# Kernel tuning notes

Measured on AMD Instinct MI355X. Metric: run time of the kernel, lower is better.

The kernel has to match this reference:

```python
import jax, jax.numpy as jnp
import numpy as np
from jax.ops import segment_sum, segment_max

N, F, H, HEADS, E, OUT = 50000, 256, 64, 4, 800000, 16


def setup_inputs() -> dict:
    key = jax.random.key(0)
    ks = jax.random.split(key, 16)
    s = 0.05
    return {
        "x": jax.random.normal(ks[0], (N, F), jnp.float32),
        "edge_index": jax.random.randint(ks[1], (2, E), 0, N, jnp.int64),
        # GCN layer params
        "W_gcn1": jax.random.normal(ks[2], (F, H), jnp.float32) * s,
        "b_gcn1": jnp.zeros((H,), jnp.float32),
        "W_gcn2": jax.random.normal(ks[3], (H, OUT), jnp.float32) * s,
        "b_gcn2": jnp.zeros((OUT,), jnp.float32),
        # GAT layer 1 (heads=HEADS, concat)
        "W_gat1": jax.random.normal(ks[4], (F, HEADS * H), jnp.float32) * s,
        "a_src1": jax.random.normal(ks[5], (HEADS, H), jnp.float32) * s,
        "a_dst1": jax.random.normal(ks[6], (HEADS, H), jnp.float32) * s,
        "b_gat1": jnp.zeros((HEADS * H,), jnp.float32),
        # GAT layer 2 (heads=1, concat=False)
        "W_gat2": jax.random.normal(ks[7], (HEADS * H, OUT), jnp.float32) * s,
        "a_src2": jax.random.normal(ks[8], (1, OUT), jnp.float32) * s,
        "a_dst2": jax.random.normal(ks[9], (1, OUT), jnp.float32) * s,
        "b_gat2": jnp.zeros((OUT,), jnp.float32),
    }


def _add_self_loops(edge_index, n):
    loop = jnp.arange(n, dtype=edge_index.dtype)
    src = jnp.concatenate([edge_index[0], loop])
    dst = jnp.concatenate([edge_index[1], loop])
    return src, dst


def _gcn(x, src, dst, norm, W, b, n):
    h = x @ W  # [N, out]
    out = segment_sum(h[src] * norm[:, None], dst, num_segments=n)
    return out + b


def _gat(x, src, dst, W, a_s, a_d, b, heads, concat, n):
    h = (x @ W).reshape(n, heads, -1)  # [N, heads, C]
    s_src = jnp.einsum("nhc,hc->nh", h, a_s)
    s_dst = jnp.einsum("nhc,hc->nh", h, a_d)
    e = jax.nn.leaky_relu(s_src[src] + s_dst[dst], 0.2)  # [Etot, heads]
    m = segment_max(e, dst, num_segments=n)               # per-dst softmax
    p = jnp.exp(e - m[dst])
    denom = segment_sum(p, dst, num_segments=n)
    alpha = p / denom[dst]
    out = segment_sum(h[src] * alpha[..., None], dst, num_segments=n)
    out = out.reshape(n, -1) if concat else out.mean(axis=1)
    return out + b


def reference(x, edge_index, W_gcn1, b_gcn1, W_gcn2, b_gcn2,
              W_gat1, a_src1, a_dst1, b_gat1,
              W_gat2, a_src2, a_dst2, b_gat2):
    n = x.shape[0]
    src, dst = _add_self_loops(edge_index, n)
    # symmetric GCN normalization on self-loop-augmented graph
    deg = segment_sum(jnp.ones_like(dst, x.dtype), dst, num_segments=n)
    dinv = jnp.where(deg > 0, jax.lax.rsqrt(deg), 0.0)
    norm = dinv[src] * dinv[dst]

    x_gcn = jax.nn.relu(_gcn(x, src, dst, norm, W_gcn1, b_gcn1, n))
    x_gcn = _gcn(x_gcn, src, dst, norm, W_gcn2, b_gcn2, n)

    x_gat = jax.nn.relu(_gat(x, src, dst, W_gat1, a_src1, a_dst1, b_gat1, HEADS, True, n))
    x_gat = _gat(x_gat, src, dst, W_gat2, a_src2, a_dst2, b_gat2, 1, False, n)

    return jnp.concatenate([x_gcn, x_gat], axis=1)
```

## Files before the change

kernel.cpp:

```cpp
#include <hip/hip_runtime.h>
#include <math.h>

#define NN     50000
#define FF     256
#define HH     64
#define NHEADS 4
#define EE     800000
#define OUTD   16

typedef __attribute__((ext_vector_type(8))) short short8;
typedef __attribute__((ext_vector_type(4))) float f32x4;

__device__ inline unsigned short f2bf(float f) {
    unsigned u = __builtin_bit_cast(unsigned, f);
    unsigned r = (u + 0x7fff + ((u >> 16) & 1)) >> 16;
    return (unsigned short)r;
}
__device__ inline float bf2f(unsigned short s) {
    unsigned u = ((unsigned)s) << 16;
    return __builtin_bit_cast(float, u);
}

__global__ void k_zero_int(int* __restrict__ p, int n) {
    int i = blockIdx.x * blockDim.x + threadIdx.x;
    if (i < n) p[i] = 0;
}

__global__ void k_count(const int* __restrict__ dst, int* __restrict__ cnt, int e) {
    int i = blockIdx.x * blockDim.x + threadIdx.x;
    if (i < e) atomicAdd(&cnt[dst[i]], 1);
}

__global__ __launch_bounds__(256) void k_scan_a(const int* __restrict__ cnt,
                                                int* __restrict__ partial, int n) {
    int i = blockIdx.x * 256 + threadIdx.x;
    int v = (i < n) ? cnt[i] : 0;
#pragma unroll
    for (int off = 32; off >= 1; off >>= 1) v += __shfl_xor(v, off, 64);
    __shared__ int ws[4];
    int wave = threadIdx.x >> 6;
    if ((threadIdx.x & 63) == 0) ws[wave] = v;
    __syncthreads();
    if (threadIdx.x == 0) partial[blockIdx.x] = ws[0] + ws[1] + ws[2] + ws[3];
}

__global__ __launch_bounds__(256) void k_scan_b(const int* __restrict__ partial,
                                                int* __restrict__ blockoff,
                                                int* __restrict__ total_out, int nb) {
    __shared__ int arr[256];
    int tid = threadIdx.x;
    arr[tid] = (tid < nb) ? partial[tid] : 0;
    __syncthreads();
#pragma unroll
    for (int off = 1; off < 256; off <<= 1) {
        int v = arr[tid];
        int add = (tid >= off) ? arr[tid - off] : 0;
        __syncthreads();
        arr[tid] = v + add;
        __syncthreads();
    }
    if (tid < nb) blockoff[tid] = arr[tid] - partial[tid];
    if (tid == 0) *total_out = arr[255];
}

__global__ __launch_bounds__(256) void k_scan_c(const int* __restrict__ cnt,
                                                const int* __restrict__ blockoff,
                                                int* __restrict__ row_start,
                                                int* __restrict__ cursor,
                                                float* __restrict__ dinv, int n) {
    __shared__ int arr[256];
    int tid = threadIdx.x;
    int i = blockIdx.x * 256 + tid;
    int c = (i < n) ? cnt[i] : 0;
    arr[tid] = c;
    __syncthreads();
#pragma unroll
    for (int off = 1; off < 256; off <<= 1) {
        int v = arr[tid];
        int add = (tid >= off) ? arr[tid - off] : 0;
        __syncthreads();
        arr[tid] = v + add;
        __syncthreads();
    }
    if (i < n) {
        int excl = arr[tid] - c + blockoff[blockIdx.x];
        row_start[i] = excl;
        cursor[i] = excl;
        dinv[i] = rsqrtf((float)(c + 1));
    }
}

__global__ void k_fill(const int* __restrict__ src, const int* __restrict__ dst,
                       int* __restrict__ cursor, int* __restrict__ col, int e) {
    int i = blockIdx.x * blockDim.x + threadIdx.x;
    if (i < e) {
        int d = dst[i];
        int pos = atomicAdd(&cursor[d], 1);
        col[pos] = src[i];
    }
}

__device__ inline void pack_one(const float* __restrict__ W,
                                unsigned short* __restrict__ bhi,
                                unsigned short* __restrict__ blo,
                                int t_, int NT, int NTOT, int TOFF, int SRC_NC) {
    int lane = t_ & 63;
    int tile = (t_ >> 6) % NT;
    int kb = (t_ >> 6) / NT;
    int q = lane >> 4, c = lane & 15;
    size_t off = ((size_t)(kb * NTOT + TOFF + tile) * 64 + lane) * 8;
#pragma unroll
    for (int j = 0; j < 8; j++) {
        float w = W[(size_t)(kb * 32 + q * 8 + j) * SRC_NC + tile * 16 + c];
        unsigned short h = f2bf(w);
        bhi[off + j] = h;
        if (blo) blo[off + j] = f2bf(w - bf2f(h));
    }
}

#define NTT 20
__global__ __launch_bounds__(256) void k_pack_all(const float* __restrict__ Wg1,
                                                  const float* __restrict__ Wgat1,
                                                  const float* __restrict__ Wg2,
                                                  const float* __restrict__ Wgat2,
                                                  unsigned short* __restrict__ bhiC,
                                                  unsigned short* __restrict__ bhiG2,
                                                  unsigned short* __restrict__ bloG2,
                                                  unsigned short* __restrict__ bhiA2,
                                                  unsigned short* __restrict__ bloA2) {
    int t = blockIdx.x * 256 + threadIdx.x;
    if (t < 2048)        pack_one(Wg1,   bhiC,  nullptr, t,         4,  NTT, 0, 64);
    else if (t < 10240)  pack_one(Wgat1, bhiC,  nullptr, t - 2048,  16, NTT, 4, 256);
    else if (t < 10368)  pack_one(Wg2,   bhiG2, bloG2,   t - 10240, 1,  1,   0, 16);
    else if (t < 10880)  pack_one(Wgat2, bhiA2, bloA2,   t - 10368, 1,  1,   0, 16);
}

__global__ __launch_bounds__(256) void mfma_gemm_fused(const float* __restrict__ A,
                                                       const unsigned short* __restrict__ Bhi,
                                                       unsigned short* __restrict__ Ch1,
                                                       unsigned short* __restrict__ Chg,
                                                       const float* __restrict__ dinv,
                                                       const float* __restrict__ a_s,
                                                       const float* __restrict__ a_d,
                                                       float* __restrict__ ssrc,
                                                       float* __restrict__ sdst,
                                                       int M) {
    const int K = 256;
    int tid = threadIdx.x;
    int w = tid >> 6, lane = tid & 63, q = lane >> 4, c = lane & 15;
    int row_base = blockIdx.x * 64 + w * 16;
    int ar = min(row_base + c, M - 1);
    const float* ap = A + (size_t)ar * K + q * 8;
    const short8* bp = (const short8*)Bhi + lane;

    f32x4 acc[NTT];
#pragma unroll
    for (int t = 0; t < NTT; t++) acc[t] = (f32x4){0.f, 0.f, 0.f, 0.f};

    for (int kb = 0; kb < 8; kb++) {
        float av[8];
        *(float4*)(av)     = *(const float4*)(ap + kb * 32);
        *(float4*)(av + 4) = *(const float4*)(ap + kb * 32 + 4);
        short8 ahi, alo;
#pragma unroll
        for (int j = 0; j < 8; j++) {
            unsigned short h = f2bf(av[j]);
            ahi[j] = (short)h;
            alo[j] = (short)f2bf(av[j] - bf2f(h));
        }
#pragma unroll
        for (int t = 0; t < NTT; t++) {
            short8 bhi = bp[(size_t)(kb * NTT + t) * 64];
            acc[t] = __builtin_amdgcn_mfma_f32_16x16x32_bf16(ahi, bhi, acc[t], 0, 0, 0);
            acc[t] = __builtin_amdgcn_mfma_f32_16x16x32_bf16(alo, bhi, acc[t], 0, 0, 0);
        }
    }

#pragma unroll
    for (int i = 0; i < 4; i++) {
        int r = row_base + q * 4 + i;
        float ss[4] = {0.f, 0.f, 0.f, 0.f};
        float sd[4] = {0.f, 0.f, 0.f, 0.f};
#pragma unroll
        for (int t = 0; t < 16; t++) {
            float v = acc[t + 4][i];
            ss[t >> 2] += v * a_s[t * 16 + c];
            sd[t >> 2] += v * a_d[t * 16 + c];
        }
#pragma unroll
        for (int h = 0; h < 4; h++) {
#pragma unroll
            for (int off = 1; off <= 8; off <<= 1) {
                ss[h] += __shfl_xor(ss[h], off, 16);
                sd[h] += __shfl_xor(sd[h], off, 16);
            }
        }
        if (c == i && r < M) {
            *(float4*)(ssrc + (size_t)r * 4) = make_float4(ss[0], ss[1], ss[2], ss[3]);
            *(float4*)(sdst + (size_t)r * 4) = make_float4(sd[0], sd[1], sd[2], sd[3]);
        }
    }

#pragma unroll
    for (int i = 0; i < 4; i++) {
        int r = row_base + q * 4 + i;
        if (r < M) {
            float sc = dinv[r];
#pragma unroll
            for (int t = 0; t < 4; t++)
                Ch1[(size_t)r * 64 + t * 16 + c] = f2bf(acc[t][i] * sc);
#pragma unroll
            for (int t = 0; t < 16; t++)
                Chg[(size_t)r * 256 + t * 16 + c] = f2bf(acc[t + 4][i]);
        }
    }
}

template <int KB, bool SCALE, bool SC2, int OFS>
__device__ inline void n16_body(int bx, int tid,
                                const unsigned short* __restrict__ A,
                                const unsigned short* __restrict__ Bhi,
                                const unsigned short* __restrict__ Blo,
                                unsigned short* __restrict__ Cbf,
                                const float* __restrict__ rowscale,
                                const float* __restrict__ a_s2,
                                const float* __restrict__ a_d2,
                                float* __restrict__ s2s,
                                float* __restrict__ s2d, int M) {
    const int K = KB * 32;
    int w = tid >> 6, lane = tid & 63, q = lane >> 4, c = lane & 15;
    int row_base = bx * 64 + w * 16;
    int ar = min(row_base + c, M - 1);
    const unsigned short* ap = A + (size_t)ar * K + q * 8;
    f32x4 acc = (f32x4){0.f, 0.f, 0.f, 0.f};
#pragma unroll
    for (int kb = 0; kb < KB; kb++) {
        short8 av = *(const short8*)(ap + kb * 32);
        size_t bo = ((size_t)kb * 64 + lane) * 8;
        short8 bh = *(const short8*)(Bhi + bo);
        short8 bl = *(const short8*)(Blo + bo);
        acc = __builtin_amdgcn_mfma_f32_16x16x32_bf16(av, bh, acc, 0, 0, 0);
        acc = __builtin_amdgcn_mfma_f32_16x16x32_bf16(av, bl, acc, 0, 0, 0);
    }
    if (SC2) {
#pragma unroll
        for (int i = 0; i < 4; i++) {
            float ps = acc[i] * a_s2[c];
            float pd = acc[i] * a_d2[c];
#pragma unroll
            for (int off = 1; off <= 8; off <<= 1) {
                ps += __shfl_xor(ps, off, 16);
                pd += __shfl_xor(pd, off, 16);
            }
            int r = row_base + q * 4 + i;
            if (c == i && r < M) {
                s2s[r] = ps;
                s2d[r] = pd;
            }
        }
    }
#pragma unroll
    for (int i = 0; i < 4; i++) {
        int r = row_base + q * 4 + i;
        if (r < M) {
            float sc = SCALE ? rowscale[r] : 1.0f;
            Cbf[((size_t)r * 16 + c) * 2 + OFS] = f2bf(acc[i] * sc);
        }
    }
}

__global__ __launch_bounds__(256) void mfma_n16_both(const unsigned short* __restrict__ Ag,
                                                     const unsigned short* __restrict__ Ac,
                                                     const unsigned short* __restrict__ bhiA2,
                                                     const unsigned short* __restrict__ bloA2,
                                                     const unsigned short* __restrict__ bhiG2,
                                                     const unsigned short* __restrict__ bloG2,
                                                     unsigned short* __restrict__ pairb,
                                                     const float* __restrict__ dinv,
                                                     const float* __restrict__ a_s2,
                                                     const float* __restrict__ a_d2,
                                                     float* __restrict__ s2s,
                                                     float* __restrict__ s2d,
                                                     int M, int GB) {
    int bx = blockIdx.x;
    if (bx < GB)
        n16_body<8, false, true, 1>(bx, threadIdx.x, Ag, bhiA2, bloA2, pairb,
                                    nullptr, a_s2, a_d2, s2s, s2d, M);
    else
        n16_body<2, true, false, 0>(bx - GB, threadIdx.x, Ac, bhiG2, bloG2, pairb,
                                    dinv, nullptr, nullptr, nullptr, nullptr, M);
}

__global__ __launch_bounds__(256) void both_agg(const unsigned short* __restrict__ hg,
                                                const unsigned short* __restrict__ h1,
                                                const int* __restrict__ rs,
                                                const int* __restrict__ col,
                                                const float* __restrict__ ssrc,
                                                const float* __restrict__ sdst,
                                                const float* __restrict__ dinv,
                                                const float* __restrict__ bgat,
                                                const float* __restrict__ bgcn,
                                                unsigned short* __restrict__ outg,
                                                unsigned short* __restrict__ outc) {
    __shared__ int s_lds[4][64];
    __shared__ float p_lds[4][64 * 4];
    int tid = threadIdx.x;
    int w = tid >> 6, lane = tid & 63;
    int wid = blockIdx.x * 4 + w;
    int hh = lane >> 4;
    int cidx = (lane & 15) * 4;
    int* sl = s_lds[w];
    float* pl = p_lds[w];

    float di = dinv[wid];
    float4 sd4 = *(const float4*)(sdst + (size_t)wid * 4);
    float sdv[4] = {sd4.x, sd4.y, sd4.z, sd4.w};
    float4 sf4 = *(const float4*)(ssrc + (size_t)wid * 4);
    float sfv[4] = {sf4.x, sf4.y, sf4.z, sf4.w};
    float psf[4];
#pragma unroll
    for (int h = 0; h < 4; h++) {
        float e = sfv[h] + sdv[h];
        e = (e >= 0.f) ? e : 0.2f * e;
        psf[h] = __expf(e);
    }
    float pse = (hh & 2) ? ((hh & 1) ? psf[3] : psf[2]) : ((hh & 1) ? psf[1] : psf[0]);
    const unsigned short* hbase = hg + lane * 4;
    ushort4 hvs = *(const ushort4*)(hbase + (size_t)wid * 256);
    float4 acc;
    acc.x = bf2f(hvs.x) * pse; acc.y = bf2f(hvs.y) * pse;
    acc.z = bf2f(hvs.z) * pse; acc.w = bf2f(hvs.w) * pse;
    float4 accc = make_float4(0.f, 0.f, 0.f, 0.f);

    float lsum[4] = {0.f, 0.f, 0.f, 0.f};
    int beg = rs[wid], end = rs[wid + 1];
    for (int j0 = beg; j0 < end; j0 += 64) {
        int cnt = min(64, end - j0);
        if (lane < cnt) {
            int sreg = col[j0 + lane];
            float4 sv = *(const float4*)(ssrc + (size_t)sreg * 4);
            float svv[4] = {sv.x, sv.y, sv.z, sv.w};
            float pv[4];
#pragma unroll
            for (int h = 0; h < 4; h++) {
                float e = svv[h] + sdv[h];
                e = (e >= 0.f) ? e : 0.2f * e;
                pv[h] = __expf(e);
                lsum[h] += pv[h];
            }
            sl[lane] = sreg;
            *(float4*)&pl[lane * 4] = make_float4(pv[0], pv[1], pv[2], pv[3]);
        }
        int e = 0;
        for (; e + 4 <= cnt; e += 4) {
            int s0 = sl[e], s1 = sl[e + 1], s2 = sl[e + 2], s3 = sl[e + 3];
            float p0 = pl[e * 4 + hh], p1 = pl[(e + 1) * 4 + hh];
            float p2 = pl[(e + 2) * 4 + hh], p3 = pl[(e + 3) * 4 + hh];
            ushort4 h0 = *(const ushort4*)(hbase + (size_t)s0 * 256);
            ushort4 h1v = *(const ushort4*)(hbase + (size_t)s1 * 256);
            ushort4 h2 = *(const ushort4*)(hbase + (size_t)s2 * 256);
            ushort4 h3 = *(const ushort4*)(hbase + (size_t)s3 * 256);
            acc.x += bf2f(h0.x) * p0; acc.y += bf2f(h0.y) * p0;
            acc.z += bf2f(h0.z) * p0; acc.w += bf2f(h0.w) * p0;
            acc.x += bf2f(h1v.x) * p1; acc.y += bf2f(h1v.y) * p1;
            acc.z += bf2f(h1v.z) * p1; acc.w += bf2f(h1v.w) * p1;
            acc.x += bf2f(h2.x) * p2; acc.y += bf2f(h2.y) * p2;
            acc.z += bf2f(h2.z) * p2; acc.w += bf2f(h2.w) * p2;
            acc.x += bf2f(h3.x) * p3; acc.y += bf2f(h3.y) * p3;
            acc.z += bf2f(h3.z) * p3; acc.w += bf2f(h3.w) * p3;
        }
        for (; e < cnt; e++) {
            int s = sl[e];
            float p = pl[e * 4 + hh];
            ushort4 hv = *(const ushort4*)(hbase + (size_t)s * 256);
            acc.x += bf2f(hv.x) * p; acc.y += bf2f(hv.y) * p;
            acc.z += bf2f(hv.z) * p; acc.w += bf2f(hv.w) * p;
        }
        int e2 = hh;
        for (; e2 + 4 < cnt; e2 += 8) {
            int sa = sl[e2], sb = sl[e2 + 4];
            ushort4 va = *(const ushort4*)(h1 + (size_t)sa * HH + cidx);
            ushort4 vb = *(const ushort4*)(h1 + (size_t)sb * HH + cidx);
            accc.x += bf2f(va.x) + bf2f(vb.x);
            accc.y += bf2f(va.y) + bf2f(vb.y);
            accc.z += bf2f(va.z) + bf2f(vb.z);
            accc.w += bf2f(va.w) + bf2f(vb.w);
        }
        if (e2 < cnt) {
            int sa = sl[e2];
            ushort4 va = *(const ushort4*)(h1 + (size_t)sa * HH + cidx);
            accc.x += bf2f(va.x); accc.y += bf2f(va.y);
            accc.z += bf2f(va.z); accc.w += bf2f(va.w);
        }
    }
#pragma unroll
    for (int h = 0; h < 4; h++) {
        float v = lsum[h];
        for (int off = 32; off >= 1; off >>= 1) v += __shfl_xor(v, off, 64);
        lsum[h] = v + psf[h];
    }
    float lt = (hh & 2) ? ((hh & 1) ? lsum[3] : lsum[2]) : ((hh & 1) ? lsum[1] : lsum[0]);
    float li = 1.0f / lt;
    float4 bv = *(const float4*)(bgat + lane * 4);
    ushort4 o;
    o.x = f2bf(fmaxf(acc.x * li + bv.x, 0.f));
    o.y = f2bf(fmaxf(acc.y * li + bv.y, 0.f));
    o.z = f2bf(fmaxf(acc.z * li + bv.z, 0.f));
    o.w = f2bf(fmaxf(acc.w * li + bv.w, 0.f));
    *(ushort4*)(outg + (size_t)wid * 256 + lane * 4) = o;
#pragma unroll
    for (int off = 16; off <= 32; off <<= 1) {
        accc.x += __shfl_xor(accc.x, off, 64);
        accc.y += __shfl_xor(accc.y, off, 64);
        accc.z += __shfl_xor(accc.z, off, 64);
        accc.w += __shfl_xor(accc.w, off, 64);
    }
    if (hh == 0) {
        ushort4 sv = *(const ushort4*)(h1 + (size_t)wid * HH + cidx);
        float4 bc = *(const float4*)(bgcn + cidx);
        ushort4 oc;
        oc.x = f2bf(fmaxf((accc.x + bf2f(sv.x)) * di + bc.x, 0.f));
        oc.y = f2bf(fmaxf((accc.y + bf2f(sv.y)) * di + bc.y, 0.f));
        oc.z = f2bf(fmaxf((accc.z + bf2f(sv.z)) * di + bc.z, 0.f));
        oc.w = f2bf(fmaxf((accc.w + bf2f(sv.w)) * di + bc.w, 0.f));
        *(ushort4*)(outc + (size_t)wid * HH + cidx) = oc;
    }
}

__global__ __launch_bounds__(256) void final_agg(const unsigned* __restrict__ hp,
                                                 const int* __restrict__ rs,
                                                 const int* __restrict__ col,
                                                 const float* __restrict__ dinv,
                                                 const float* __restrict__ s2s,
                                                 const float* __restrict__ s2d,
                                                 const float* __restrict__ bg2,
                                                 const float* __restrict__ bga2,
                                                 float* __restrict__ out) {
    int t = blockIdx.x * 256 + threadIdx.x;
    int node = t >> 4;
    int c = t & 15;
    float di = dinv[node];
    float sd = s2d[node];
    float es = s2s[node] + sd;
    es = (es >= 0.f) ? es : 0.2f * es;
    float psf = __expf(es);
    unsigned pvs = hp[(size_t)node * 16 + c];
    float accg = bf2f((unsigned short)pvs);
    float acca = bf2f((unsigned short)(pvs >> 16)) * psf;
    float lp = 0.f;
    int beg = rs[node], end = rs[node + 1];
    for (int j0 = beg; j0 < end; j0 += 16) {
        int cnt = min(16, end - j0);
        int sreg = 0;
        float pr = 0.f;
        if (c < cnt) {
            sreg = col[j0 + c];
            float e = s2s[sreg] + sd;
            e = (e >= 0.f) ? e : 0.2f * e;
            pr = __expf(e);
            lp += pr;
        }
        for (int e = 0; e < cnt; e += 4) {
            int si[4];
            float pi[4];
#pragma unroll
            for (int u = 0; u < 4; u++) {
                si[u] = __shfl(sreg, (e + u) & 15, 16);
                pi[u] = __shfl(pr, (e + u) & 15, 16);
            }
            unsigned hv[4];
#pragma unroll
            for (int u = 0; u < 4; u++) hv[u] = hp[(size_t)si[u] * 16 + c];
#pragma unroll
            for (int u = 0; u < 4; u++) {
                if (e + u < cnt) {
                    accg += bf2f((unsigned short)hv[u]);
                    acca += bf2f((unsigned short)(hv[u] >> 16)) * pi[u];
                }
            }
        }
    }
    for (int off = 8; off >= 1; off >>= 1) lp += __shfl_xor(lp, off, 16);
    float l = lp + psf;
    out[(size_t)node * 32 + c] = accg * di + bg2[c];
    out[(size_t)node * 32 + 16 + c] = acca / l + bga2[c];
}

extern "C" void kernel_launch(void* const* d_in, const int* in_sizes, int n_in,
                              void* d_out, int out_size, void* d_ws, size_t ws_size,
                              hipStream_t stream) {
    const float* x      = (const float*)d_in[0];
    const int*   ei     = (const int*)d_in[1];
    const float* Wg1    = (const float*)d_in[2];
    const float* bg1    = (const float*)d_in[3];
    const float* Wg2    = (const float*)d_in[4];
    const float* bg2    = (const float*)d_in[5];
    const float* Wgat1  = (const float*)d_in[6];
    const float* a_src1 = (const float*)d_in[7];
    const float* a_dst1 = (const float*)d_in[8];
    const float* bgat1  = (const float*)d_in[9];
    const float* Wgat2  = (const float*)d_in[10];
    const float* a_src2 = (const float*)d_in[11];
    const float* a_dst2 = (const float*)d_in[12];
    const float* bgat2  = (const float*)d_in[13];
    float* out = (float*)d_out;

    const int* e_src = ei;
    const int* e_dst = ei + EE;

    char* wsb = (char*)d_ws;
    size_t o = 0;
    auto alloc = [&](size_t bytes) -> void* {
        void* p = wsb + o;
        o += (bytes + 255) & ~(size_t)255;
        return p;
    };
    float* dinv            = (float*)alloc(NN * 4);
    float* ssrc1           = (float*)alloc((size_t)NN * 16);
    float* sdst1           = (float*)alloc((size_t)NN * 16);
    unsigned short* h1b    = (unsigned short*)alloc((size_t)NN * HH * 2);
    unsigned short* xg1    = (unsigned short*)alloc((size_t)NN * HH * 2);
    unsigned short* hgb    = (unsigned short*)alloc((size_t)NN * 256 * 2);
    unsigned short* xgat1  = (unsigned short*)alloc((size_t)NN * 256 * 2);
    unsigned short* pairb  = (unsigned short*)alloc((size_t)NN * 16 * 4);
    float* s2src           = (float*)alloc(NN * 4);
    float* s2dst           = (float*)alloc(NN * 4);
    unsigned short* bhiC   = (unsigned short*)alloc((size_t)8 * NTT * 512 * 2);
    unsigned short* bhiG2  = (unsigned short*)alloc(64 * 16 * 2);
    unsigned short* bloG2  = (unsigned short*)alloc(64 * 16 * 2);
    unsigned short* bhiA2  = (unsigned short*)alloc(256 * 16 * 2);
    unsigned short* bloA2  = (unsigned short*)alloc(256 * 16 * 2);
    int* cnt               = (int*)alloc(NN * 4);
    int* rowstart          = (int*)alloc((NN + 1) * 4);
    int* cursor            = (int*)alloc(NN * 4);
    int* colarr            = (int*)alloc((size_t)EE * 4);
    int* partial           = (int*)alloc(256 * 4);
    int* blockoff          = (int*)alloc(256 * 4);

    const int TB = 256;
    const int NB = (NN + 255) / 256;
    k_zero_int<<<(NN + TB - 1) / TB, TB, 0, stream>>>(cnt, NN);
    k_count<<<(EE + TB - 1) / TB, TB, 0, stream>>>(e_dst, cnt, EE);
    k_scan_a<<<NB, TB, 0, stream>>>(cnt, partial, NN);
    k_scan_b<<<1, TB, 0, stream>>>(partial, blockoff, rowstart + NN, NB);
    k_scan_c<<<NB, TB, 0, stream>>>(cnt, blockoff, rowstart, cursor, dinv, NN);
    k_fill<<<(EE + TB - 1) / TB, TB, 0, stream>>>(e_src, e_dst, cursor, colarr, EE);
    k_pack_all<<<(10880 + TB - 1) / TB, TB, 0, stream>>>(Wg1, Wgat1, Wg2, Wgat2,
                                                         bhiC, bhiG2, bloG2,
                                                         bhiA2, bloA2);

    const int GB = (NN + 63) / 64;
    const int G16 = (NN * 16) / 256;

    mfma_gemm_fused<<<GB, TB, 0, stream>>>(x, bhiC, h1b, hgb, dinv,
                                           a_src1, a_dst1, ssrc1, sdst1, NN);

    both_agg<<<NN / 4, TB, 0, stream>>>(hgb, h1b, rowstart, colarr, ssrc1, sdst1,
                                        dinv, bgat1, bg1, xgat1, xg1);

    mfma_n16_both<<<2 * GB, TB, 0, stream>>>(xgat1, xg1, bhiA2, bloA2, bhiG2, bloG2,
                                             pairb, dinv, a_src2, a_dst2,
                                             s2src, s2dst, NN, GB);

    final_agg<<<G16, TB, 0, stream>>>((const unsigned*)pairb, rowstart, colarr, dinv,
                                      s2src, s2dst, bg2, bgat2, out);
}
```

Measured before the change: 355.2 us.

## Fuse CSR build and weight packing into one persistent kernel with grid barriers

Merges the seven preprocessing kernels (zero, count, three-stage scan, fill, weight pack) into a single 512-block persistent kernel. The stages are separated by atomic-flag grid barriers and a decoupled partial-sum lookback, with flags cleared by a memset. The goal is to remove per-launch overhead and the inter-kernel gaps. The GAT aggregation inner loop is also unrolled from 4 to 8 neighbors so more gathers are in flight at once. The spin barriers assume all 512 blocks are co-resident on the device; if they are not, the kernel deadlocks. The single-kernel stages also get less parallelism than separate launches.

```diff
diff --git a/kernel.cpp b/kernel.cpp
--- a/kernel.cpp
+++ b/kernel.cpp
@@ -19,85 +19,6 @@
 __device__ inline float bf2f(unsigned short s) {
     unsigned u = ((unsigned)s) << 16;
     return __builtin_bit_cast(float, u);
-}
-
-__global__ void k_zero_int(int* __restrict__ p, int n) {
-    int i = blockIdx.x * blockDim.x + threadIdx.x;
-    if (i < n) p[i] = 0;
-}
-
-__global__ void k_count(const int* __restrict__ dst, int* __restrict__ cnt, int e) {
-    int i = blockIdx.x * blockDim.x + threadIdx.x;
-    if (i < e) atomicAdd(&cnt[dst[i]], 1);
-}
-
-__global__ __launch_bounds__(256) void k_scan_a(const int* __restrict__ cnt,
-                                                int* __restrict__ partial, int n) {
-    int i = blockIdx.x * 256 + threadIdx.x;
-    int v = (i < n) ? cnt[i] : 0;
-#pragma unroll
-    for (int off = 32; off >= 1; off >>= 1) v += __shfl_xor(v, off, 64);
-    __shared__ int ws[4];
-    int wave = threadIdx.x >> 6;
-    if ((threadIdx.x & 63) == 0) ws[wave] = v;
-    __syncthreads();
-    if (threadIdx.x == 0) partial[blockIdx.x] = ws[0] + ws[1] + ws[2] + ws[3];
-}
-
-__global__ __launch_bounds__(256) void k_scan_b(const int* __restrict__ partial,
-                                                int* __restrict__ blockoff,
-                                                int* __restrict__ total_out, int nb) {
-    __shared__ int arr[256];
-    int tid = threadIdx.x;
-    arr[tid] = (tid < nb) ? partial[tid] : 0;
-    __syncthreads();
-#pragma unroll
-    for (int off = 1; off < 256; off <<= 1) {
-        int v = arr[tid];
-        int add = (tid >= off) ? arr[tid - off] : 0;
-        __syncthreads();
-        arr[tid] = v + add;
-        __syncthreads();
-    }
-    if (tid < nb) blockoff[tid] = arr[tid] - partial[tid];
-    if (tid == 0) *total_out = arr[255];
-}
-
-__global__ __launch_bounds__(256) void k_scan_c(const int* __restrict__ cnt,
-                                                const int* __restrict__ blockoff,
-                                                int* __restrict__ row_start,
-                                                int* __restrict__ cursor,
-                                                float* __restrict__ dinv, int n) {
-    __shared__ int arr[256];
-    int tid = threadIdx.x;
-    int i = blockIdx.x * 256 + tid;
-    int c = (i < n) ? cnt[i] : 0;
-    arr[tid] = c;
-    __syncthreads();
-#pragma unroll
-    for (int off = 1; off < 256; off <<= 1) {
-        int v = arr[tid];
-        int add = (tid >= off) ? arr[tid - off] : 0;
-        __syncthreads();
-        arr[tid] = v + add;
-        __syncthreads();
-    }
-    if (i < n) {
-        int excl = arr[tid] - c + blockoff[blockIdx.x];
-        row_start[i] = excl;
-        cursor[i] = excl;
-        dinv[i] = rsqrtf((float)(c + 1));
-    }
-}
-
-__global__ void k_fill(const int* __restrict__ src, const int* __restrict__ dst,
-                       int* __restrict__ cursor, int* __restrict__ col, int e) {
-    int i = blockIdx.x * blockDim.x + threadIdx.x;
-    if (i < e) {
-        int d = dst[i];
-        int pos = atomicAdd(&cursor[d], 1);
-        col[pos] = src[i];
-    }
 }
 
 __device__ inline void pack_one(const float* __restrict__ W,
@@ -119,20 +40,105 @@
 }
 
 #define NTT 20
-__global__ __launch_bounds__(256) void k_pack_all(const float* __restrict__ Wg1,
-                                                  const float* __restrict__ Wgat1,
-                                                  const float* __restrict__ Wg2,
-                                                  const float* __restrict__ Wgat2,
-                                                  unsigned short* __restrict__ bhiC,
-                                                  unsigned short* __restrict__ bhiG2,
-                                                  unsigned short* __restrict__ bloG2,
-                                                  unsigned short* __restrict__ bhiA2,
-                                                  unsigned short* __restrict__ bloA2) {
-    int t = blockIdx.x * 256 + threadIdx.x;
-    if (t < 2048)        pack_one(Wg1,   bhiC,  nullptr, t,         4,  NTT, 0, 64);
-    else if (t < 10240)  pack_one(Wgat1, bhiC,  nullptr, t - 2048,  16, NTT, 4, 256);
-    else if (t < 10368)  pack_one(Wg2,   bhiG2, bloG2,   t - 10240, 1,  1,   0, 16);
-    else if (t < 10880)  pack_one(Wgat2, bhiA2, bloA2,   t - 10368, 1,  1,   0, 16);
+#define CSRB 512
+
+__global__ __launch_bounds__(256) void k_csr_build(
+        const int* __restrict__ esrc, const int* __restrict__ edst,
+        const float* __restrict__ Wg1, const float* __restrict__ Wgat1,
+        const float* __restrict__ Wg2, const float* __restrict__ Wgat2,
+        unsigned short* __restrict__ bhiC,
+        unsigned short* __restrict__ bhiG2, unsigned short* __restrict__ bloG2,
+        unsigned short* __restrict__ bhiA2, unsigned short* __restrict__ bloA2,
+        int* __restrict__ cnt, int* __restrict__ rowstart,
+        int* __restrict__ cursor, float* __restrict__ dinv,
+        int* __restrict__ col, int* __restrict__ flags, int* __restrict__ partial) {
+    const int tid = threadIdx.x;
+    const int bx = blockIdx.x;
+    const int gid = bx * 256 + tid;
+    const int gsz = CSRB * 256;
+    const int NCH = (NN + 255) / 256;
+
+    for (int i = gid; i < NN; i += gsz) atomicExch(&cnt[i], 0);
+    if (gid < 2048)                       pack_one(Wg1,   bhiC,  nullptr, gid,          4,  NTT, 0, 64);
+    else if (gid < 10240)                 pack_one(Wgat1, bhiC,  nullptr, gid - 2048,   16, NTT, 4, 256);
+    else if (gid < 10368)                 pack_one(Wg2,   bhiG2, bloG2,   gid - 10240,  1,  1,   0, 16);
+    else if (gid < 10880)                 pack_one(Wgat2, bhiA2, bloA2,   gid - 10368,  1,  1,   0, 16);
+    __syncthreads();
+    if (tid == 0) {
+        __threadfence();
+        atomicAdd(&flags[0], 1);
+        while (atomicAdd(&flags[0], 0) < CSRB) __builtin_amdgcn_s_sleep(2);
+    }
+    __syncthreads();
+    __threadfence();
+
+    for (int e = gid; e < EE; e += gsz) atomicAdd(&cnt[edst[e]], 1);
+    __syncthreads();
+    if (tid == 0) {
+        __threadfence();
+        atomicAdd(&flags[1], 1);
+        while (atomicAdd(&flags[1], 0) < CSRB) __builtin_amdgcn_s_sleep(2);
+    }
+    __syncthreads();
+    __threadfence();
+
+    __shared__ int arr[256];
+    __shared__ int poff[256];
+    if (bx < NCH) {
+        int i = bx * 256 + tid;
+        int c = (i < NN) ? atomicAdd(&cnt[i], 0) : 0;
+        arr[tid] = c;
+        __syncthreads();
+#pragma unroll
+        for (int off = 1; off < 256; off <<= 1) {
+            int v = arr[tid];
+            int add = (tid >= off) ? arr[tid - off] : 0;
+            __syncthreads();
+            arr[tid] = v + add;
+            __syncthreads();
+        }
+        int incl = arr[tid];
+        int ctotal = arr[255];
+        if (tid == 0) atomicExch(&partial[bx], ctotal + 1);
+        int pv = 0;
+        if (tid < NCH) {
+            while ((pv = atomicAdd(&partial[tid], 0)) == 0) __builtin_amdgcn_s_sleep(2);
+            pv -= 1;
+        }
+        poff[tid] = pv;
+        __syncthreads();
+#pragma unroll
+        for (int off = 1; off < 256; off <<= 1) {
+            int v = poff[tid];
+            int add = (tid >= off) ? poff[tid - off] : 0;
+            __syncthreads();
+            poff[tid] = v + add;
+            __syncthreads();
+        }
+        int blockoff = (bx > 0) ? poff[bx - 1] : 0;
+        if (i < NN) {
+            int excl = incl - c + blockoff;
+            rowstart[i] = excl;
+            atomicExch(&cursor[i], excl);
+            dinv[i] = rsqrtf((float)(c + 1));
+        }
+        if (bx == 0 && tid == 0) rowstart[NN] = EE;
+        __syncthreads();
+        if (tid == 0) {
+            __threadfence();
+            atomicAdd(&flags[2], 1);
+        }
+    }
+    if (tid == 0) {
+        while (atomicAdd(&flags[2], 0) < NCH) __builtin_amdgcn_s_sleep(2);
+    }
+    __syncthreads();
+    __threadfence();
+    for (int e = gid; e < EE; e += gsz) {
+        int d = edst[e];
+        int pos = atomicAdd(&cursor[d], 1);
+        col[pos] = esrc[e];
+    }
 }
 
 __global__ __launch_bounds__(256) void mfma_gemm_fused(const float* __restrict__ A,
@@ -352,22 +358,23 @@
             *(float4*)&pl[lane * 4] = make_float4(pv[0], pv[1], pv[2], pv[3]);
         }
         int e = 0;
-        for (; e + 4 <= cnt; e += 4) {
-            int s0 = sl[e], s1 = sl[e + 1], s2 = sl[e + 2], s3 = sl[e + 3];
-            float p0 = pl[e * 4 + hh], p1 = pl[(e + 1) * 4 + hh];
-            float p2 = pl[(e + 2) * 4 + hh], p3 = pl[(e + 3) * 4 + hh];
-            ushort4 h0 = *(const ushort4*)(hbase + (size_t)s0 * 256);
-            ushort4 h1v = *(const ushort4*)(hbase + (size_t)s1 * 256);
-            ushort4 h2 = *(const ushort4*)(hbase + (size_t)s2 * 256);
-            ushort4 h3 = *(const ushort4*)(hbase + (size_t)s3 * 256);
-            acc.x += bf2f(h0.x) * p0; acc.y += bf2f(h0.y) * p0;
-            acc.z += bf2f(h0.z) * p0; acc.w += bf2f(h0.w) * p0;
-            acc.x += bf2f(h1v.x) * p1; acc.y += bf2f(h1v.y) * p1;
-            acc.z += bf2f(h1v.z) * p1; acc.w += bf2f(h1v.w) * p1;
-            acc.x += bf2f(h2.x) * p2; acc.y += bf2f(h2.y) * p2;
-            acc.z += bf2f(h2.z) * p2; acc.w += bf2f(h2.w) * p2;
-            acc.x += bf2f(h3.x) * p3; acc.y += bf2f(h3.y) * p3;
-            acc.z += bf2f(h3.z) * p3; acc.w += bf2f(h3.w) * p3;
+        for (; e + 8 <= cnt; e += 8) {
+            int sv0[8]; float pv0[8]; ushort4 hv[8];
+#pragma unroll
+            for (int u = 0; u < 8; u++) {
+                sv0[u] = sl[e + u];
+                pv0[u] = pl[(e + u) * 4 + hh];
+            }
+#pragma unroll
+            for (int u = 0; u < 8; u++)
+                hv[u] = *(const ushort4*)(hbase + (size_t)sv0[u] * 256);
+#pragma unroll
+            for (int u = 0; u < 8; u++) {
+                acc.x += bf2f(hv[u].x) * pv0[u];
+                acc.y += bf2f(hv[u].y) * pv0[u];
+                acc.z += bf2f(hv[u].z) * pv0[u];
+                acc.w += bf2f(hv[u].w) * pv0[u];
+            }
         }
         for (; e < cnt; e++) {
             int s = sl[e];
@@ -515,6 +522,8 @@
         o += (bytes + 255) & ~(size_t)255;
         return p;
     };
+    int* flags             = (int*)alloc(64);
+    int* partial           = (int*)alloc(256 * 4);
     float* dinv            = (float*)alloc(NN * 4);
     float* ssrc1           = (float*)alloc((size_t)NN * 16);
     float* sdst1           = (float*)alloc((size_t)NN * 16);
@@ -534,20 +543,14 @@
     int* rowstart          = (int*)alloc((NN + 1) * 4);
     int* cursor            = (int*)alloc(NN * 4);
     int* colarr            = (int*)alloc((size_t)EE * 4);
-    int* partial           = (int*)alloc(256 * 4);
-    int* blockoff          = (int*)alloc(256 * 4);
 
     const int TB = 256;
-    const int NB = (NN + 255) / 256;
-    k_zero_int<<<(NN + TB - 1) / TB, TB, 0, stream>>>(cnt, NN);
-    k_count<<<(EE + TB - 1) / TB, TB, 0, stream>>>(e_dst, cnt, EE);
-    k_scan_a<<<NB, TB, 0, stream>>>(cnt, partial, NN);
-    k_scan_b<<<1, TB, 0, stream>>>(partial, blockoff, rowstart + NN, NB);
-    k_scan_c<<<NB, TB, 0, stream>>>(cnt, blockoff, rowstart, cursor, dinv, NN);
-    k_fill<<<(EE + TB - 1) / TB, TB, 0, stream>>>(e_src, e_dst, cursor, colarr, EE);
-    k_pack_all<<<(10880 + TB - 1) / TB, TB, 0, stream>>>(Wg1, Wgat1, Wg2, Wgat2,
-                                                         bhiC, bhiG2, bloG2,
-                                                         bhiA2, bloA2);
+    hipMemsetAsync(d_ws, 0, 2048, stream);
+
+    k_csr_build<<<CSRB, TB, 0, stream>>>(e_src, e_dst, Wg1, Wgat1, Wg2, Wgat2,
+                                         bhiC, bhiG2, bloG2, bhiA2, bloA2,
+                                         cnt, rowstart, cursor, dinv, colarr,
+                                         flags, partial);
 
     const int GB = (NN + 63) / 64;
     const int G16 = (NN * 16) / 256;
```

After: 533.2 us. +50.1%, slower.
